# Kernel tuning notes

Hardware: AMD Instinct MI355X
Metric: run time of the kernel (lower is better)

Reference implementation:

```python
import jax, jax.numpy as jnp
import numpy as np

D = 1024      # embedding_dim
H = 16        # num_heads
HD = D // H   # head_dim = 64
B = 2
L = 2048


def setup_inputs() -> dict:
    key = jax.random.key(0)
    k_x, k_q, k_k, k_v, k_o = jax.random.split(key, 5)
    s = 1.0 / np.sqrt(D)
    return {
        "embedded": jax.random.normal(k_x, (B, L, D), dtype=jnp.float32),
        "Wq": jax.random.uniform(k_q, (H, D, HD), jnp.float32, -s, s),  # per-head q proj
        "Wk": jax.random.uniform(k_k, (H, D, HD), jnp.float32, -s, s),
        "Wv": jax.random.uniform(k_v, (H, D, HD), jnp.float32, -s, s),
        "Wo": jax.random.uniform(k_o, (D, D), jnp.float32, -s, s),      # output proj [in, out]
    }


def reference(embedded, Wq, Wk, Wv, Wo):
    # Batched per-head projections: [B,L,D] x [H,D,hd] -> [B,H,L,hd]
    q = jnp.einsum('bld,hde->bhle', embedded, Wq)
    k = jnp.einsum('bld,hde->bhle', embedded, Wk)
    v = jnp.einsum('bld,hde->bhle', embedded, Wv)
    scores = jnp.einsum('bhqe,bhke->bhqk', q, k) / jnp.sqrt(jnp.float32(HD))
    Lq = embedded.shape[1]
    causal = jnp.tril(jnp.ones((Lq, Lq), dtype=bool))  # allow j <= i
    scores = jnp.where(causal[None, None], scores, jnp.float32(-jnp.inf))
    attn = jax.nn.softmax(scores, axis=-1)
    out = jnp.einsum('bhqk,bhke->bhqe', attn, v)          # [B,H,L,hd]
    concat = out.transpose(0, 2, 1, 3).reshape(embedded.shape[0], Lq, H * HD)  # head order matches torch cat
    return concat @ Wo
```

## Files before the change

kernel.cpp:

```cpp
#include <hip/hip_runtime.h>
#include <hip/hip_bf16.h>


#define GM 4096
#define GK 1024
#define GL 2048
#define GH 16

typedef __attribute__((ext_vector_type(8))) short bf16x8;
typedef __attribute__((ext_vector_type(4))) float f32x4;
typedef __attribute__((ext_vector_type(16))) float f32x16;
typedef unsigned short u16;

__device__ __forceinline__ u16 bfu(float x) {
    __hip_bfloat16 h = __float2bfloat16(x);
    return *reinterpret_cast<u16*>(&h);
}
__device__ __forceinline__ unsigned pack_bf16(float a, float b) {
    return ((unsigned)bfu(b) << 16) | bfu(a);
}
__device__ __forceinline__ unsigned pack_trunc(float a, float b) {
    return __builtin_amdgcn_perm(__float_as_uint(b), __float_as_uint(a), 0x07060302u);
}
__device__ __forceinline__ void gl_lds16(const void* g, void* l) {
    __builtin_amdgcn_global_load_lds(
        (__attribute__((address_space(1))) void*)(g),
        (__attribute__((address_space(3))) void*)(l),
        16, 0, 0);
}
__device__ __forceinline__ float fexp2(float x) {
#if __has_builtin(__builtin_amdgcn_exp2f)
    return __builtin_amdgcn_exp2f(x);
#else
    return __expf(x * 0.6931471805599453f);
#endif
}
__device__ __forceinline__ int sig5(int c) {
    return (c & 3) | (((c >> 3) & 1) << 2) | (((c >> 2) & 1) << 3) | (c & 16);
}

#define SM_SCALE 0.1803368801111204f
#define RESCALE_THR 8.0f

__global__ __launch_bounds__(256) void cast_bf16(
    const float* __restrict__ src, u16* __restrict__ dst, int n8)
{
    int i = blockIdx.x * 256 + threadIdx.x;
    if (i >= n8) return;
    float4 v0 = reinterpret_cast<const float4*>(src)[i * 2];
    float4 v1 = reinterpret_cast<const float4*>(src)[i * 2 + 1];
    uint4 o;
    o.x = pack_bf16(v0.x, v0.y);
    o.y = pack_bf16(v0.z, v0.w);
    o.z = pack_bf16(v1.x, v1.y);
    o.w = pack_bf16(v1.z, v1.w);
    reinterpret_cast<uint4*>(dst)[i] = o;
}

__global__ __launch_bounds__(256) void transpose_qkv(
    const float* __restrict__ Wq, const float* __restrict__ Wk,
    const float* __restrict__ Wv, u16* __restrict__ dst)
{
    __shared__ float T[64][65];
    const int t = threadIdx.x;
    const int z = blockIdx.z;
    const int r0 = blockIdx.x * 64;
    const float* s = (z < 16 ? Wq : (z < 32 ? Wk : Wv)) + (size_t)(z & 15) * 65536;
    u16* d = dst + (size_t)z * 65536;
#pragma unroll
    for (int i = 0; i < 4; ++i) {
        int idx = i * 256 + t;
        int row = idx >> 4, col = (idx & 15) * 4;
        float4 v = *reinterpret_cast<const float4*>(&s[(size_t)(r0 + row) * 64 + col]);
        T[row][col] = v.x; T[row][col + 1] = v.y;
        T[row][col + 2] = v.z; T[row][col + 3] = v.w;
    }
    __syncthreads();
#pragma unroll
    for (int i = 0; i < 4; ++i) {
        int idx = i * 256 + t;
        int oc = idx >> 4, ok = (idx & 15) * 4;
        ushort4 o;
        o.x = bfu(T[ok][oc]);     o.y = bfu(T[ok + 1][oc]);
        o.z = bfu(T[ok + 2][oc]); o.w = bfu(T[ok + 3][oc]);
        *reinterpret_cast<ushort4*>(&d[(size_t)oc * 1024 + r0 + ok]) = o;
    }
}

__global__ __launch_bounds__(256) void transpose_bf16(
    const float* __restrict__ src, u16* __restrict__ dst, int R, int C)
{
    __shared__ float T[64][65];
    const int t = threadIdx.x;
    const int r0 = blockIdx.x * 64, c0 = blockIdx.y * 64;
#pragma unroll
    for (int i = 0; i < 4; ++i) {
        int idx = i * 256 + t;
        int row = idx >> 4, col = (idx & 15) * 4;
        float4 v = *reinterpret_cast<const float4*>(&src[(size_t)(r0 + row) * C + c0 + col]);
        T[row][col] = v.x; T[row][col + 1] = v.y;
        T[row][col + 2] = v.z; T[row][col + 3] = v.w;
    }
    __syncthreads();
#pragma unroll
    for (int i = 0; i < 4; ++i) {
        int idx = i * 256 + t;
        int oc = idx >> 4, ok = (idx & 15) * 4;
        ushort4 o;
        o.x = bfu(T[ok][oc]);     o.y = bfu(T[ok + 1][oc]);
        o.z = bfu(T[ok + 2][oc]); o.w = bfu(T[ok + 3][oc]);
        *reinterpret_cast<ushort4*>(&dst[(size_t)(c0 + oc) * R + r0 + ok]) = o;
    }
}

__global__ __launch_bounds__(256) void gemm_mfma(
    const u16* __restrict__ A, const u16* __restrict__ Bt,
    float* __restrict__ Cf, u16* __restrict__ Cq, u16* __restrict__ Ck,
    u16* __restrict__ Cvt, int fused)
{
    __shared__ u16 As[128 * 64];
    __shared__ u16 Bs[64 * 64];

    const int tid  = threadIdx.x;
    const int lane = tid & 63;
    const int w    = tid >> 6;
    const int g    = lane >> 4;
    const int c15  = lane & 15;
    const int wr   = w >> 1, wc = w & 1;
    const int m0   = blockIdx.x * 128;
    const int by   = blockIdx.y;

    const u16* Bb = Bt + (size_t)by * (64 * 1024);
    const int srow8  = lane >> 3;
    const int schunk = lane & 7;

    f32x4 acc[4][2];
#pragma unroll
    for (int mf = 0; mf < 4; ++mf)
#pragma unroll
        for (int nf = 0; nf < 2; ++nf) acc[mf][nf] = f32x4{0.f, 0.f, 0.f, 0.f};

    for (int k0 = 0; k0 < GK; k0 += 64) {
#pragma unroll
        for (int c = 0; c < 4; ++c) {
            int row = c * 32 + w * 8 + srow8;
            int gc = schunk ^ (row & 7);
            gl_lds16(A + (size_t)(m0 + row) * GK + k0 + gc * 8,
                     As + c * 2048 + w * 512);
        }
#pragma unroll
        for (int c = 0; c < 2; ++c) {
            int row = c * 32 + w * 8 + srow8;
            int gc = schunk ^ (row & 7);
            gl_lds16(Bb + (size_t)row * GK + k0 + gc * 8,
                     Bs + c * 2048 + w * 512);
        }
        __syncthreads();

#pragma unroll
        for (int kc = 0; kc < 2; ++kc) {
            bf16x8 a[4], b[2];
#pragma unroll
            for (int mf = 0; mf < 4; ++mf) {
                int row = wr * 64 + mf * 16 + c15;
                int ch = (kc * 4 + g) ^ (row & 7);
                a[mf] = *reinterpret_cast<const bf16x8*>(As + row * 64 + ch * 8);
            }
#pragma unroll
            for (int nf = 0; nf < 2; ++nf) {
                int row = wc * 32 + nf * 16 + c15;
                int ch = (kc * 4 + g) ^ (row & 7);
                b[nf] = *reinterpret_cast<const bf16x8*>(Bs + row * 64 + ch * 8);
            }
#pragma unroll
            for (int mf = 0; mf < 4; ++mf)
#pragma unroll
                for (int nf = 0; nf < 2; ++nf)
                    acc[mf][nf] = __builtin_amdgcn_mfma_f32_16x16x32_bf16(
                        a[mf], b[nf], acc[mf][nf], 0, 0, 0);
        }
        __syncthreads();
    }

    if (!fused) {
#pragma unroll
        for (int mf = 0; mf < 4; ++mf) {
            int m = m0 + wr * 64 + mf * 16 + g * 4;
#pragma unroll
            for (int nf = 0; nf < 2; ++nf) {
                int n = by * 64 + wc * 32 + nf * 16 + c15;
#pragma unroll
                for (int r = 0; r < 4; ++r)
                    Cf[(size_t)(m + r) * 1024 + n] = acc[mf][nf][r];
            }
        }
        return;
    }
    const int proj = by >> 4;
    const int head = by & 15;
    const int b = m0 >> 11, l0 = m0 & 2047;
    if (proj < 2) {
        u16* C = proj ? Ck : Cq;
        const float qs = proj ? 1.f : SM_SCALE;
        const size_t bh = ((size_t)(b * GH + head)) * GL * 64;
#pragma unroll
        for (int mf = 0; mf < 4; ++mf) {
            int l = l0 + wr * 64 + mf * 16 + g * 4;
#pragma unroll
            for (int nf = 0; nf < 2; ++nf) {
                int n = wc * 32 + nf * 16 + c15;
#pragma unroll
                for (int r = 0; r < 4; ++r)
                    C[bh + (size_t)(l + r) * 64 + n] = bfu(acc[mf][nf][r] * qs);
            }
        }
    } else {
        const size_t bh = ((size_t)(b * GH + head)) * 64 * GL;
#pragma unroll
        for (int mf = 0; mf < 4; ++mf) {
            int l = l0 + wr * 64 + mf * 16 + g * 4;
#pragma unroll
            for (int nf = 0; nf < 2; ++nf) {
                int n = wc * 32 + nf * 16 + c15;
                ushort4 o;
                o.x = bfu(acc[mf][nf][0]); o.y = bfu(acc[mf][nf][1]);
                o.z = bfu(acc[mf][nf][2]); o.w = bfu(acc[mf][nf][3]);
                *reinterpret_cast<ushort4*>(&Cvt[bh + (size_t)n * GL + l]) = o;
            }
        }
    }
}

template <bool DOMASK>
__device__ __forceinline__ void attn_step32(
    const u16* __restrict__ Kt, const u16* __restrict__ Vt,
    const bf16x8* qf, int qrow, int j0, int qi, int hi,
    float& m_run, float& l_run, f32x16& o0, f32x16& o1)
{
    const int swz = qi & 7;

    f32x16 s0 = {0.f,0.f,0.f,0.f,0.f,0.f,0.f,0.f,0.f,0.f,0.f,0.f,0.f,0.f,0.f,0.f};
    f32x16 s1 = s0;
#pragma unroll
    for (int dc = 0; dc < 4; ++dc) {
        const int ch = ((dc * 2 + hi) ^ swz) * 8;
        bf16x8 kf0 = *reinterpret_cast<const bf16x8*>(Kt + qi * 64 + ch);
        bf16x8 kf1 = *reinterpret_cast<const bf16x8*>(Kt + (32 + qi) * 64 + ch);
        s0 = __builtin_amdgcn_mfma_f32_32x32x16_bf16(kf0, qf[dc], s0, 0, 0, 0);
        s1 = __builtin_amdgcn_mfma_f32_32x32x16_bf16(kf1, qf[dc], s1, 0, 0, 0);
    }

    if (DOMASK) {
#pragma unroll
        for (int r = 0; r < 16; ++r) {
            const int kl = (r & 3) + (((r >> 2) & 1) << 2) + (hi << 3)
                         + (((r >> 3) & 1) << 4);
            if (j0 + kl > qrow)      s0[r] = -__builtin_inff();
            if (j0 + 32 + kl > qrow) s1[r] = -__builtin_inff();
        }
    }

    float ma = fmaxf(s0[0], s0[1]), mb = fmaxf(s0[2], s0[3]);
    float mc = fmaxf(s1[0], s1[1]), md = fmaxf(s1[2], s1[3]);
#pragma unroll
    for (int r = 4; r < 16; r += 4) {
        ma = fmaxf(ma, fmaxf(s0[r], s0[r + 1]));
        mb = fmaxf(mb, fmaxf(s0[r + 2], s0[r + 3]));
        mc = fmaxf(mc, fmaxf(s1[r], s1[r + 1]));
        md = fmaxf(md, fmaxf(s1[r + 2], s1[r + 3]));
    }
    float mx = fmaxf(fmaxf(ma, mb), fmaxf(mc, md));
    mx = fmaxf(mx, __shfl_xor(mx, 32));

    if (!__all(mx <= m_run + RESCALE_THR)) {
        const float mnew = fmaxf(m_run, mx);
        const float scl  = fexp2(m_run - mnew);
        l_run *= scl;
        o0 *= scl;
        o1 *= scl;
        m_run = mnew;
    }

    float rsum = 0.f;
    unsigned pk0[8], pk1[8];
#pragma unroll
    for (int p = 0; p < 8; ++p) {
        float a = fexp2(s0[2 * p] - m_run), b = fexp2(s0[2 * p + 1] - m_run);
        float c = fexp2(s1[2 * p] - m_run), d = fexp2(s1[2 * p + 1] - m_run);
        rsum += (a + b) + (c + d);
        pk0[p] = pack_trunc(a, b);
        pk1[p] = pack_trunc(c, d);
    }
    rsum += __shfl_xor(rsum, 32);
    l_run += rsum;

    __builtin_amdgcn_s_setprio(1);
#pragma unroll
    for (int j2 = 0; j2 < 4; ++j2) {
        const int J4 = (j2 & 1) * 4;
        uint4 uu;
        if (j2 < 2) { uu.x = pk0[J4]; uu.y = pk0[J4 + 1]; uu.z = pk0[J4 + 2]; uu.w = pk0[J4 + 3]; }
        else        { uu.x = pk1[J4]; uu.y = pk1[J4 + 1]; uu.z = pk1[J4 + 2]; uu.w = pk1[J4 + 3]; }
        bf16x8 pf = __builtin_bit_cast(bf16x8, uu);
        const int chv = ((j2 * 2 + hi) ^ swz) * 8;
        bf16x8 vf0 = *reinterpret_cast<const bf16x8*>(Vt + qi * 64 + chv);
        bf16x8 vf1 = *reinterpret_cast<const bf16x8*>(Vt + (32 + qi) * 64 + chv);
        o0 = __builtin_amdgcn_mfma_f32_32x32x16_bf16(vf0, pf, o0, 0, 0, 0);
        o1 = __builtin_amdgcn_mfma_f32_32x32x16_bf16(vf1, pf, o1, 0, 0, 0);
    }
    __builtin_amdgcn_s_setprio(0);
}

__global__ __launch_bounds__(256) void attn_mfma(
    const u16* __restrict__ qg, const u16* __restrict__ kg,
    const u16* __restrict__ vtg, u16* __restrict__ og)
{
    __shared__ u16 Ks[2][64 * 64];
    __shared__ u16 Vs[2][64 * 64];

    const int tid  = threadIdx.x;
    const int lane = tid & 63;
    const int w    = tid >> 6;
    const int qi   = lane & 31;
    const int hi   = lane >> 5;

    const int bid  = blockIdx.x;
    const int j    = bid & 255;
    const int half = bid >> 8;
    const int bh   = j & 31;
    const int s    = j >> 5;
    const int c    = half ? (15 - s) : s;

    const size_t qkb  = (size_t)bh * GL * 64;
    const size_t vtbo = (size_t)bh * 64 * GL;

    const int qrow = c * 128 + w * 32 + qi;
    bf16x8 qf[4];
#pragma unroll
    for (int dc = 0; dc < 4; ++dc)
        qf[dc] = *reinterpret_cast<const bf16x8*>(
            qg + qkb + (size_t)qrow * 64 + dc * 16 + hi * 8);

    const int lrow = lane >> 3;
    const int lch  = lane & 7;

    auto stage = [&](int t, u16* kd, u16* vd) {
#pragma unroll
        for (int cc = 0; cc < 2; ++cc) {
            const int row = cc * 32 + w * 8 + lrow;
            const int gc  = lch ^ (row & 7);
            const int ksrc = t * 64 + (row & 32) + sig5(row & 31);
            gl_lds16(kg + qkb + (size_t)ksrc * 64 + gc * 8,
                     kd + (cc * 32 + w * 8) * 64);
            gl_lds16(vtg + vtbo + (size_t)row * GL + t * 64 + gc * 8,
                     vd + (cc * 32 + w * 8) * 64);
        }
    };

    float m_run = -__builtin_inff(), l_run = 0.f;
    f32x16 o0 = {0.f,0.f,0.f,0.f,0.f,0.f,0.f,0.f,0.f,0.f,0.f,0.f,0.f,0.f,0.f,0.f};
    f32x16 o1 = o0;

    stage(0, Ks[0], Vs[0]);
    __syncthreads();

    for (int tt = 0; tt < c; ++tt) {
        stage(2 * tt + 1, Ks[1], Vs[1]);
        attn_step32<false>(Ks[0], Vs[0], qf, qrow, (2 * tt) * 64, qi, hi,
                           m_run, l_run, o0, o1);
        __syncthreads();
        stage(2 * tt + 2, Ks[0], Vs[0]);
        attn_step32<false>(Ks[1], Vs[1], qf, qrow, (2 * tt + 1) * 64, qi, hi,
                           m_run, l_run, o0, o1);
        __syncthreads();
    }
    stage(2 * c + 1, Ks[1], Vs[1]);
    if (w < 2)
        attn_step32<true>(Ks[0], Vs[0], qf, qrow, (2 * c) * 64, qi, hi,
                          m_run, l_run, o0, o1);
    else
        attn_step32<false>(Ks[0], Vs[0], qf, qrow, (2 * c) * 64, qi, hi,
                           m_run, l_run, o0, o1);
    __syncthreads();
    if (w >= 2)
        attn_step32<true>(Ks[1], Vs[1], qf, qrow, (2 * c + 1) * 64, qi, hi,
                          m_run, l_run, o0, o1);

    const int b = bh >> 4, h = bh & 15;
    const float inv = 1.f / l_run;
    u16* obase = og + ((size_t)(b * GL + qrow)) * 1024 + h * 64 + 4 * hi;
#pragma unroll
    for (int rq = 0; rq < 4; ++rq) {
        ushort4 w0, w1;
        w0.x = bfu(o0[4 * rq] * inv);     w0.y = bfu(o0[4 * rq + 1] * inv);
        w0.z = bfu(o0[4 * rq + 2] * inv); w0.w = bfu(o0[4 * rq + 3] * inv);
        *reinterpret_cast<ushort4*>(obase + 8 * rq) = w0;
        w1.x = bfu(o1[4 * rq] * inv);     w1.y = bfu(o1[4 * rq + 1] * inv);
        w1.z = bfu(o1[4 * rq + 2] * inv); w1.w = bfu(o1[4 * rq + 3] * inv);
        *reinterpret_cast<ushort4*>(obase + 32 + 8 * rq) = w1;
    }
}

extern "C" void kernel_launch(void* const* d_in, const int* in_sizes, int n_in,
                              void* d_out, int out_size, void* d_ws, size_t ws_size,
                              hipStream_t stream) {
    const float* emb = (const float*)d_in[0];
    const float* Wq  = (const float*)d_in[1];
    const float* Wk  = (const float*)d_in[2];
    const float* Wv  = (const float*)d_in[3];
    const float* Wo  = (const float*)d_in[4];
    float* out = (float*)d_out;

    char* ws = (char*)d_ws;
    u16* qb   = (u16*)(ws);
    u16* kb   = (u16*)(ws + ( 8u << 20));
    u16* vtb  = (u16*)(ws + (16u << 20));
    u16* ab   = (u16*)(ws + (24u << 20));
    u16* embb = (u16*)(ws + (32u << 20));
    u16* wqt  = (u16*)(ws + (40u << 20));
    u16* wot  = (u16*)(ws + (46u << 20));

    dim3 blk(256);

    cast_bf16<<<dim3(2048), blk, 0, stream>>>(emb, embb, GM * GK / 8);
    transpose_qkv<<<dim3(16, 1, 48), blk, 0, stream>>>(Wq, Wk, Wv, wqt);
    transpose_bf16<<<dim3(16, 16, 1), blk, 0, stream>>>(Wo, wot, 1024, 1024);

    gemm_mfma<<<dim3(GM / 128, 48), blk, 0, stream>>>(
        embb, wqt, nullptr, qb, kb, vtb, 1);

    attn_mfma<<<dim3(512), blk, 0, stream>>>(qb, kb, vtb, ab);

    gemm_mfma<<<dim3(GM / 128, 16), blk, 0, stream>>>(
        ab, wot, out, nullptr, nullptr, nullptr, 0);
}
```

Measured before the change: 109.9 us.

## Triple-buffer K/V tiles with vmcnt waits and a new XOR swizzle

Replaces the double-buffered K/V LDS staging in the attention kernel with a three-slot ring buffer. Each step waits on outstanding global loads with explicit vmcnt counts and a single barrier, so tile i+2 is prefetched while tile i is computed. It also changes the LDS swizzle so the XOR key depends on row bits 3-5 as well as 0-2, with a different key for the upper 32 rows, aimed at reducing bank conflicts on the fragment reads. This raises LDS use from 32KB to 48KB per block, which may lower occupancy.

```diff
diff --git a/kernel.cpp b/kernel.cpp
--- a/kernel.cpp
+++ b/kernel.cpp
@@ -38,6 +38,17 @@
 __device__ __forceinline__ int sig5(int c) {
     return (c & 3) | (((c >> 3) & 1) << 2) | (((c >> 2) & 1) << 3) | (c & 16);
 }
+__device__ __forceinline__ int rswz(int row) {
+    return (row & 7) ^ ((row >> 3) & 7);
+}
+
+#define WAITV4() do { asm volatile("s_waitcnt vmcnt(4)" ::: "memory"); \
+                      __builtin_amdgcn_sched_barrier(0); } while (0)
+#define WAITV0() do { asm volatile("s_waitcnt vmcnt(0)" ::: "memory"); \
+                      __builtin_amdgcn_sched_barrier(0); } while (0)
+#define BARRIER() do { __builtin_amdgcn_sched_barrier(0); \
+                       __builtin_amdgcn_s_barrier(); \
+                       __builtin_amdgcn_sched_barrier(0); } while (0)
 
 #define SM_SCALE 0.1803368801111204f
 #define RESCALE_THR 8.0f
@@ -237,15 +248,16 @@
     const bf16x8* qf, int qrow, int j0, int qi, int hi,
     float& m_run, float& l_run, f32x16& o0, f32x16& o1)
 {
-    const int swz = qi & 7;
+    const int ks0 = rswz(qi);
+    const int ks1 = ks0 ^ 4;
 
     f32x16 s0 = {0.f,0.f,0.f,0.f,0.f,0.f,0.f,0.f,0.f,0.f,0.f,0.f,0.f,0.f,0.f,0.f};
     f32x16 s1 = s0;
 #pragma unroll
     for (int dc = 0; dc < 4; ++dc) {
-        const int ch = ((dc * 2 + hi) ^ swz) * 8;
-        bf16x8 kf0 = *reinterpret_cast<const bf16x8*>(Kt + qi * 64 + ch);
-        bf16x8 kf1 = *reinterpret_cast<const bf16x8*>(Kt + (32 + qi) * 64 + ch);
+        const int x = dc * 2 + hi;
+        bf16x8 kf0 = *reinterpret_cast<const bf16x8*>(Kt + qi * 64 + ((x ^ ks0) * 8));
+        bf16x8 kf1 = *reinterpret_cast<const bf16x8*>(Kt + (32 + qi) * 64 + ((x ^ ks1) * 8));
         s0 = __builtin_amdgcn_mfma_f32_32x32x16_bf16(kf0, qf[dc], s0, 0, 0, 0);
         s1 = __builtin_amdgcn_mfma_f32_32x32x16_bf16(kf1, qf[dc], s1, 0, 0, 0);
     }
@@ -302,9 +314,9 @@
         if (j2 < 2) { uu.x = pk0[J4]; uu.y = pk0[J4 + 1]; uu.z = pk0[J4 + 2]; uu.w = pk0[J4 + 3]; }
         else        { uu.x = pk1[J4]; uu.y = pk1[J4 + 1]; uu.z = pk1[J4 + 2]; uu.w = pk1[J4 + 3]; }
         bf16x8 pf = __builtin_bit_cast(bf16x8, uu);
-        const int chv = ((j2 * 2 + hi) ^ swz) * 8;
-        bf16x8 vf0 = *reinterpret_cast<const bf16x8*>(Vt + qi * 64 + chv);
-        bf16x8 vf1 = *reinterpret_cast<const bf16x8*>(Vt + (32 + qi) * 64 + chv);
+        const int x = j2 * 2 + hi;
+        bf16x8 vf0 = *reinterpret_cast<const bf16x8*>(Vt + qi * 64 + ((x ^ ks0) * 8));
+        bf16x8 vf1 = *reinterpret_cast<const bf16x8*>(Vt + (32 + qi) * 64 + ((x ^ ks1) * 8));
         o0 = __builtin_amdgcn_mfma_f32_32x32x16_bf16(vf0, pf, o0, 0, 0, 0);
         o1 = __builtin_amdgcn_mfma_f32_32x32x16_bf16(vf1, pf, o1, 0, 0, 0);
     }
@@ -315,8 +327,8 @@
     const u16* __restrict__ qg, const u16* __restrict__ kg,
     const u16* __restrict__ vtg, u16* __restrict__ og)
 {
-    __shared__ u16 Ks[2][64 * 64];
-    __shared__ u16 Vs[2][64 * 64];
+    __shared__ u16 Ksh[3][64 * 64];
+    __shared__ u16 Vsh[3][64 * 64];
 
     const int tid  = threadIdx.x;
     const int lane = tid & 63;
@@ -341,19 +353,16 @@
         qf[dc] = *reinterpret_cast<const bf16x8*>(
             qg + qkb + (size_t)qrow * 64 + dc * 16 + hi * 8);
 
-    const int lrow = lane >> 3;
-    const int lch  = lane & 7;
-
     auto stage = [&](int t, u16* kd, u16* vd) {
 #pragma unroll
-        for (int cc = 0; cc < 2; ++cc) {
-            const int row = cc * 32 + w * 8 + lrow;
-            const int gc  = lch ^ (row & 7);
+        for (int c8 = 0; c8 < 2; ++c8) {
+            const int row = w * 16 + c8 * 8 + (lane >> 3);
+            const int gc  = (lane & 7) ^ rswz(row);
             const int ksrc = t * 64 + (row & 32) + sig5(row & 31);
             gl_lds16(kg + qkb + (size_t)ksrc * 64 + gc * 8,
-                     kd + (cc * 32 + w * 8) * 64);
+                     kd + (w * 16 + c8 * 8) * 64);
             gl_lds16(vtg + vtbo + (size_t)row * GL + t * 64 + gc * 8,
-                     vd + (cc * 32 + w * 8) * 64);
+                     vd + (w * 16 + c8 * 8) * 64);
         }
     };
 
@@ -361,30 +370,35 @@
     f32x16 o0 = {0.f,0.f,0.f,0.f,0.f,0.f,0.f,0.f,0.f,0.f,0.f,0.f,0.f,0.f,0.f,0.f};
     f32x16 o1 = o0;
 
-    stage(0, Ks[0], Vs[0]);
-    __syncthreads();
-
-    for (int tt = 0; tt < c; ++tt) {
-        stage(2 * tt + 1, Ks[1], Vs[1]);
-        attn_step32<false>(Ks[0], Vs[0], qf, qrow, (2 * tt) * 64, qi, hi,
-                           m_run, l_run, o0, o1);
-        __syncthreads();
-        stage(2 * tt + 2, Ks[0], Vs[0]);
-        attn_step32<false>(Ks[1], Vs[1], qf, qrow, (2 * tt + 1) * 64, qi, hi,
-                           m_run, l_run, o0, o1);
-        __syncthreads();
-    }
-    stage(2 * c + 1, Ks[1], Vs[1]);
-    if (w < 2)
-        attn_step32<true>(Ks[0], Vs[0], qf, qrow, (2 * c) * 64, qi, hi,
-                          m_run, l_run, o0, o1);
-    else
-        attn_step32<false>(Ks[0], Vs[0], qf, qrow, (2 * c) * 64, qi, hi,
-                           m_run, l_run, o0, o1);
-    __syncthreads();
-    if (w >= 2)
-        attn_step32<true>(Ks[1], Vs[1], qf, qrow, (2 * c + 1) * 64, qi, hi,
-                          m_run, l_run, o0, o1);
+    const int nt = 2 * c + 2;
+    u16 *k0 = Ksh[0], *k1 = Ksh[1], *k2 = Ksh[2];
+    u16 *v0 = Vsh[0], *v1 = Vsh[1], *v2 = Vsh[2];
+
+    stage(0, k0, v0);
+    stage(1, k1, v1);
+
+    for (int i = 0; i < nt; ++i) {
+        if (i < nt - 1) WAITV4();
+        else            WAITV0();
+        BARRIER();
+        if (i + 2 < nt) stage(i + 2, k2, v2);
+
+        const int j0 = i * 64;
+        if (i < 2 * c) {
+            attn_step32<false>(k0, v0, qf, qrow, j0, qi, hi, m_run, l_run, o0, o1);
+        } else if (i == 2 * c) {
+            if (w < 2)
+                attn_step32<true>(k0, v0, qf, qrow, j0, qi, hi, m_run, l_run, o0, o1);
+            else
+                attn_step32<false>(k0, v0, qf, qrow, j0, qi, hi, m_run, l_run, o0, o1);
+        } else {
+            if (w >= 2)
+                attn_step32<true>(k0, v0, qf, qrow, j0, qi, hi, m_run, l_run, o0, o1);
+        }
+
+        u16* tk = k0; k0 = k1; k1 = k2; k2 = tk;
+        u16* tv = v0; v0 = v1; v1 = v2; v2 = tv;
+    }
 
     const int b = bh >> 4, h = bh & 15;
     const float inv = 1.f / l_run;
```

Measured after the change: 115.3 us. +4.9%, slower.
